# Kernel tuning notes

Hardware: AMD Instinct MI355X
Metric: run time of the kernel (lower is better)

Reference implementation:

```python
import jax, jax.numpy as jnp
import numpy as np

B, T, S_ENC, D, H, E, K = 4, 1024, 64, 1024, 16, 8, 2
DK = D // H
HID = 4 * D
NEG = -65504.0
EPS = 1e-5


def rmsnorm(x, w):
    return w * (x * jax.lax.rsqrt(jnp.mean(x * x, axis=-1, keepdims=True) + EPS))


def mha(xq, xk, xv, mask, wq, wk, wv, wo):
    # linear (no bias): y = x @ W.T
    q = jnp.einsum('bsd,ed->bse', xq, wq).reshape(xq.shape[0], -1, H, DK).transpose(0, 2, 1, 3)
    k = jnp.einsum('bsd,ed->bse', xk, wk).reshape(xk.shape[0], -1, H, DK).transpose(0, 2, 1, 3)
    v = jnp.einsum('bsd,ed->bse', xv, wv).reshape(xv.shape[0], -1, H, DK).transpose(0, 2, 1, 3)
    scores = jnp.einsum('bhqd,bhkd->bhqk', q, k) / jnp.sqrt(jnp.float32(DK))
    scores = jnp.where(mask[:, None, :, :] == 0, NEG, scores)
    attn = jax.nn.softmax(scores, axis=-1)
    out = jnp.einsum('bhqk,bhkd->bhqd', attn, v)
    out = out.transpose(0, 2, 1, 3).reshape(xq.shape[0], -1, D)
    return jnp.einsum('bsd,ed->bse', out, wo)


def moe_ffn(x, gate_w, exp_w1, exp_w2, sh_w1, sh_w2):
    b, s, d = x.shape
    xf = x.reshape(-1, d)                                     # [N, D]
    # shared expert
    sh = jnp.einsum('nd,hd->nh', xf, sh_w1)
    sh = jax.nn.silu(sh)
    sh = jnp.einsum('nh,dh->nd', sh, sh_w2)
    # gating
    logits = jnp.einsum('nd,ed->ne', xf, gate_w)              # [N, E]
    topk_vals, topk_idx = jax.lax.top_k(logits, K)
    topk_gates = jax.nn.softmax(topk_vals, axis=-1)
    n = xf.shape[0]
    gates = jnp.zeros((n, E), dtype=xf.dtype).at[jnp.arange(n)[:, None], topk_idx].set(topk_gates)
    # all experts computed densely (as in the torch code), then gated
    h = jnp.einsum('nd,ehd->neh', xf, exp_w1)                 # [N, E, 4D]
    h = jax.nn.silu(h)
    eo = jnp.einsum('neh,edh->ned', h, exp_w2)                # [N, E, D]
    sel = jnp.einsum('ned,ne->nd', eo, gates)
    return (sh + sel).reshape(b, s, d)


def setup_inputs() -> dict:
    key = jax.random.key(0)
    ks = jax.random.split(key, 16)
    sd = 1.0 / np.sqrt(D)
    inp = {
        'x': jax.random.normal(ks[0], (B, T, D), jnp.float32),
        'encoder_output': jax.random.normal(ks[1], (B, S_ENC, D), jnp.float32),
        'tgt_mask': jnp.tril(jnp.ones((T, T), jnp.int32))[None].repeat(B, 0),
        'src_mask': jnp.ones((B, T, S_ENC), jnp.int32),
        'norm1_w': jnp.ones((D,), jnp.float32),
        'norm2_w': jnp.ones((D,), jnp.float32),
        'norm3_w': jnp.ones((D,), jnp.float32),
        'sa_wq': jax.random.normal(ks[2], (D, D), jnp.float32) * sd,
        'sa_wk': jax.random.normal(ks[3], (D, D), jnp.float32) * sd,
        'sa_wv': jax.random.normal(ks[4], (D, D), jnp.float32) * sd,
        'sa_wo': jax.random.normal(ks[5], (D, D), jnp.float32) * sd,
        'ca_wq': jax.random.normal(ks[6], (D, D), jnp.float32) * sd,
        'ca_wk': jax.random.normal(ks[7], (D, D), jnp.float32) * sd,
        'ca_wv': jax.random.normal(ks[8], (D, D), jnp.float32) * sd,
        'ca_wo': jax.random.normal(ks[9], (D, D), jnp.float32) * sd,
        'gate_w': jax.random.normal(ks[10], (E, D), jnp.float32) * 0.02,
        'exp_w1': jax.random.normal(ks[11], (E, HID, D), jnp.float32) * sd,
        'exp_w2': jax.random.normal(ks[12], (E, D, HID), jnp.float32) / np.sqrt(HID),
        'sh_w1': jax.random.normal(ks[13], (HID, D), jnp.float32) * sd,
        'sh_w2': jax.random.normal(ks[14], (D, HID), jnp.float32) / np.sqrt(HID),
    }
    return inp


def reference(x, encoder_output, tgt_mask, src_mask, norm1_w, norm2_w, norm3_w,
              sa_wq, sa_wk, sa_wv, sa_wo, ca_wq, ca_wk, ca_wv, ca_wo,
              gate_w, exp_w1, exp_w2, sh_w1, sh_w2):
    xn = rmsnorm(x, norm1_w)
    h = x + mha(xn, xn, xn, tgt_mask, sa_wq, sa_wk, sa_wv, sa_wo)
    hn = rmsnorm(h, norm2_w)
    h = h + mha(hn, encoder_output, encoder_output, src_mask, ca_wq, ca_wk, ca_wv, ca_wo)
    hn = rmsnorm(h, norm3_w)
    return h + moe_ffn(hn, gate_w, exp_w1, exp_w2, sh_w1, sh_w2)
```

## Files before the change

kernel.cpp:

```cpp
#include <hip/hip_runtime.h>
#include <hip/hip_bf16.h>
#include <cstdint>
#include <cstddef>
#include <math.h>

typedef __attribute__((ext_vector_type(8))) short bf16x8;
typedef __attribute__((ext_vector_type(4))) float f32x4;
typedef __attribute__((ext_vector_type(4))) short s16x4;

static __device__ __forceinline__ short f2bf(float f) {
  union { __hip_bfloat16 b; short s; } u;
  u.b = __float2bfloat16(f);
  return u.s;
}

static __device__ __forceinline__ float bf2f(short s) {
  union { unsigned u; float f; } v;
  v.u = ((unsigned)(unsigned short)s) << 16;
  return v.f;
}

static __device__ __forceinline__ void gload_lds16(const short* g, short* l) {
  __builtin_amdgcn_global_load_lds((const __attribute__((address_space(1))) void*)g,
                                   (__attribute__((address_space(3))) void*)l,
                                   16, 0, 0);
}

__global__ __launch_bounds__(256) void cvt_k(const float* __restrict__ src,
                                             short* __restrict__ dst, long n4) {
  long i = (long)blockIdx.x * blockDim.x + threadIdx.x;
  long stride = (long)gridDim.x * blockDim.x;
  for (; i < n4; i += stride) {
    float4 v = ((const float4*)src)[i];
    s16x4 o;
    o.x = f2bf(v.x); o.y = f2bf(v.y); o.z = f2bf(v.z); o.w = f2bf(v.w);
    ((s16x4*)dst)[i] = o;
  }
}

__global__ __launch_bounds__(256) void cvt2_k(const float* __restrict__ src,
                                              short* __restrict__ hi,
                                              short* __restrict__ lo, long n4) {
  long i = (long)blockIdx.x * blockDim.x + threadIdx.x;
  long stride = (long)gridDim.x * blockDim.x;
  for (; i < n4; i += stride) {
    float4 v = ((const float4*)src)[i];
    s16x4 h, l;
    h.x = f2bf(v.x); l.x = f2bf(v.x - bf2f(h.x));
    h.y = f2bf(v.y); l.y = f2bf(v.y - bf2f(h.y));
    h.z = f2bf(v.z); l.z = f2bf(v.z - bf2f(h.z));
    h.w = f2bf(v.w); l.w = f2bf(v.w - bf2f(h.w));
    ((s16x4*)hi)[i] = h;
    ((s16x4*)lo)[i] = l;
  }
}

__global__ __launch_bounds__(256) void rms2_k(const float* __restrict__ x,
                                              const float* __restrict__ w,
                                              short* __restrict__ hi,
                                              short* __restrict__ lo) {
  const int row = blockIdx.x, tid = threadIdx.x;
  const float* xr = x + (size_t)row * 1024;
  float4 v = *(const float4*)&xr[tid * 4];
  float ss = v.x * v.x + v.y * v.y + v.z * v.z + v.w * v.w;
#pragma unroll
  for (int off = 32; off; off >>= 1) ss += __shfl_down(ss, off);
  __shared__ float red[4];
  if ((tid & 63) == 0) red[tid >> 6] = ss;
  __syncthreads();
  float rs = rsqrtf((red[0] + red[1] + red[2] + red[3]) * (1.f / 1024.f) + 1e-5f);
  float4 wv = *(const float4*)&w[tid * 4];
  float o0 = v.x * rs * wv.x, o1 = v.y * rs * wv.y;
  float o2 = v.z * rs * wv.z, o3 = v.w * rs * wv.w;
  s16x4 h, l;
  h.x = f2bf(o0); l.x = f2bf(o0 - bf2f(h.x));
  h.y = f2bf(o1); l.y = f2bf(o1 - bf2f(h.y));
  h.z = f2bf(o2); l.z = f2bf(o2 - bf2f(h.z));
  h.w = f2bf(o3); l.w = f2bf(o3 - bf2f(h.w));
  const size_t ib = (size_t)row * 1024 + tid * 4;
  *(s16x4*)&hi[ib] = h;
  *(s16x4*)&lo[ib] = l;
}

__global__ __launch_bounds__(256) void rms_k(const float* __restrict__ x,
                                             const float* __restrict__ w,
                                             short* __restrict__ obf) {
  const int row = blockIdx.x, tid = threadIdx.x;
  const float* xr = x + (size_t)row * 1024;
  float4 v = *(const float4*)&xr[tid * 4];
  float ss = v.x * v.x + v.y * v.y + v.z * v.z + v.w * v.w;
#pragma unroll
  for (int off = 32; off; off >>= 1) ss += __shfl_down(ss, off);
  __shared__ float red[4];
  if ((tid & 63) == 0) red[tid >> 6] = ss;
  __syncthreads();
  float rs = rsqrtf((red[0] + red[1] + red[2] + red[3]) * (1.f / 1024.f) + 1e-5f);
  float4 wv = *(const float4*)&w[tid * 4];
  s16x4 ob;
  ob.x = f2bf(v.x * rs * wv.x); ob.y = f2bf(v.y * rs * wv.y);
  ob.z = f2bf(v.z * rs * wv.z); ob.w = f2bf(v.w * rs * wv.w);
  *(s16x4*)&obf[(size_t)row * 1024 + tid * 4] = ob;
}

template <int EPI>
__global__ __launch_bounds__(256)
void gemm3_k(const short* __restrict__ Ah, const short* __restrict__ Al,
             const short* __restrict__ Bh, const short* __restrict__ Bl,
             float* __restrict__ C, const float* __restrict__ resid,
             int M, int N, int K) {
  __shared__ short sAh[128 * 32];
  __shared__ short sAl[128 * 32];
  __shared__ short sBh[128 * 32];
  __shared__ short sBl[128 * 32];

  const int tid = threadIdx.x;
  const int bn = blockIdx.x, bm = blockIdx.y;
  const int lane = tid & 63, wv = tid >> 6;
  const int rch = lane >> 2, cch = (lane & 3) << 3;
  const int wr = wv >> 1, wc = wv & 1;
  const int lr = lane & 15, lg = lane >> 4;
  const int c0 = wv * 2, c1 = wv * 2 + 1;

  const int ra0 = bm * 128 + c0 * 16 + rch;
  const int ra1 = bm * 128 + c1 * 16 + rch;
  const int rb0 = bn * 128 + c0 * 16 + rch, rb1 = bn * 128 + c1 * 16 + rch;

  f32x4 acc[4][4];
#pragma unroll
  for (int m = 0; m < 4; m++)
#pragma unroll
    for (int n = 0; n < 4; n++) acc[m][n] = (f32x4){0.f, 0.f, 0.f, 0.f};

  const int nk = K >> 5;
  for (int kt = 0; kt < nk; ++kt) {
    __syncthreads();
    const int colk = (kt << 5) + cch;
    gload_lds16(Ah + (size_t)ra0 * K + colk, &sAh[c0 * 512]);
    gload_lds16(Ah + (size_t)ra1 * K + colk, &sAh[c1 * 512]);
    gload_lds16(Al + (size_t)ra0 * K + colk, &sAl[c0 * 512]);
    gload_lds16(Al + (size_t)ra1 * K + colk, &sAl[c1 * 512]);
    gload_lds16(Bh + (size_t)rb0 * K + colk, &sBh[c0 * 512]);
    gload_lds16(Bh + (size_t)rb1 * K + colk, &sBh[c1 * 512]);
    gload_lds16(Bl + (size_t)rb0 * K + colk, &sBl[c0 * 512]);
    gload_lds16(Bl + (size_t)rb1 * K + colk, &sBl[c1 * 512]);
    __syncthreads();
    bf16x8 ah[4], al[4], bh[4], bl[4];
#pragma unroll
    for (int m = 0; m < 4; m++) {
      const int o = (wr * 64 + m * 16 + lr) * 32 + lg * 8;
      ah[m] = *(const bf16x8*)&sAh[o];
      al[m] = *(const bf16x8*)&sAl[o];
    }
#pragma unroll
    for (int n = 0; n < 4; n++) {
      const int o = (wc * 64 + n * 16 + lr) * 32 + lg * 8;
      bh[n] = *(const bf16x8*)&sBh[o];
      bl[n] = *(const bf16x8*)&sBl[o];
    }
#pragma unroll
    for (int m = 0; m < 4; m++)
#pragma unroll
      for (int n = 0; n < 4; n++) {
        acc[m][n] = __builtin_amdgcn_mfma_f32_16x16x32_bf16(ah[m], bh[n], acc[m][n], 0, 0, 0);
        acc[m][n] = __builtin_amdgcn_mfma_f32_16x16x32_bf16(al[m], bh[n], acc[m][n], 0, 0, 0);
        acc[m][n] = __builtin_amdgcn_mfma_f32_16x16x32_bf16(ah[m], bl[n], acc[m][n], 0, 0, 0);
      }
  }

  const int cbase = bn * 128 + wc * 64;
#pragma unroll
  for (int m = 0; m < 4; m++) {
    const int rl = bm * 128 + wr * 64 + m * 16 + lg * 4;
#pragma unroll
    for (int n = 0; n < 4; n++) {
      f32x4 v = acc[m][n];
      const int col = cbase + n * 16 + lr;
#pragma unroll
      for (int j = 0; j < 4; j++) {
        const size_t idx = (size_t)(rl + j) * N + col;
        if (EPI == 0) C[idx] = v[j];
        else C[idx] = v[j] + resid[idx];
      }
    }
  }
}

__global__ __launch_bounds__(256)
void attn32t_k(const float* __restrict__ Q, int ldq,
               const float* __restrict__ K, int ldk,
               const float* __restrict__ V, int ldv,
               short* __restrict__ Oh, short* __restrict__ Ol, int ldo,
               int Tq, int Tkv, int causal, float scale) {
  __shared__ float sQt[64][68];
  __shared__ float sKP[64][68];
  __shared__ float sV[64][68];

  const int idx = blockIdx.x;
  const int qb = 15 - (idx >> 6);
  const int h = (idx >> 2) & 15;
  const int b = idx & 3;
  const int tid = threadIdx.x;
  const int tx = tid & 15, ty = tid >> 4;
  const int hoff = h * 64;
  const int srow = tid >> 2;
  const int scol = (tid & 3) * 4;

  {
    const float* qp = &Q[(size_t)(b * Tq + qb * 64 + srow) * ldq + hoff + scol];
#pragma unroll
    for (int j = 0; j < 4; j++) {
      float4 v = *(const float4*)&qp[j * 16];
      sQt[scol + j * 16 + 0][srow] = v.x;
      sQt[scol + j * 16 + 1][srow] = v.y;
      sQt[scol + j * 16 + 2][srow] = v.z;
      sQt[scol + j * 16 + 3][srow] = v.w;
    }
  }

  float o[4][4];
  float m_run[4], l_run[4];
#pragma unroll
  for (int i = 0; i < 4; i++) {
    m_run[i] = -1e30f; l_run[i] = 0.f;
#pragma unroll
    for (int j = 0; j < 4; j++) o[i][j] = 0.f;
  }

  const int ntiles = causal ? (qb + 1) : (Tkv >> 6);
  for (int kt = 0; kt < ntiles; ++kt) {
    __syncthreads();
    {
      const float* kp = &K[(size_t)(b * Tkv + kt * 64 + srow) * ldk + hoff + scol];
      const float* vp = &V[(size_t)(b * Tkv + kt * 64 + srow) * ldv + hoff + scol];
#pragma unroll
      for (int j = 0; j < 4; j++) {
        float4 kv = *(const float4*)&kp[j * 16];
        sKP[scol + j * 16 + 0][srow] = kv.x;
        sKP[scol + j * 16 + 1][srow] = kv.y;
        sKP[scol + j * 16 + 2][srow] = kv.z;
        sKP[scol + j * 16 + 3][srow] = kv.w;
        *(float4*)&sV[srow][scol + j * 16] = *(const float4*)&vp[j * 16];
      }
    }
    __syncthreads();

    float s[4][4];
#pragma unroll
    for (int i = 0; i < 4; i++)
#pragma unroll
      for (int j = 0; j < 4; j++) s[i][j] = 0.f;
#pragma unroll 2
    for (int d = 0; d < 64; d++) {
      float4 qv = *(const float4*)&sQt[d][ty * 4];
      float4 kv = *(const float4*)&sKP[d][tx * 4];
      float qa[4] = {qv.x, qv.y, qv.z, qv.w};
      float ka[4] = {kv.x, kv.y, kv.z, kv.w};
#pragma unroll
      for (int i = 0; i < 4; i++)
#pragma unroll
        for (int j = 0; j < 4; j++) s[i][j] += qa[i] * ka[j];
    }

#pragma unroll
    for (int i = 0; i < 4; i++) {
      const int qg = qb * 64 + ty * 4 + i;
      float tmax = -1e30f;
#pragma unroll
      for (int j = 0; j < 4; j++) {
        float xv = s[i][j] * scale;
        if (causal && (kt * 64 + tx * 4 + j) > qg) xv = -1e30f;
        s[i][j] = xv;
        tmax = fmaxf(tmax, xv);
      }
      tmax = fmaxf(tmax, __shfl_xor(tmax, 1));
      tmax = fmaxf(tmax, __shfl_xor(tmax, 2));
      tmax = fmaxf(tmax, __shfl_xor(tmax, 4));
      tmax = fmaxf(tmax, __shfl_xor(tmax, 8));
      const float m_new = fmaxf(m_run[i], tmax);
      const float alpha = __expf(m_run[i] - m_new);
      float tsum = 0.f;
#pragma unroll
      for (int j = 0; j < 4; j++) {
        float e = (s[i][j] <= -1e29f) ? 0.f : __expf(s[i][j] - m_new);
        s[i][j] = e; tsum += e;
      }
      tsum += __shfl_xor(tsum, 1);
      tsum += __shfl_xor(tsum, 2);
      tsum += __shfl_xor(tsum, 4);
      tsum += __shfl_xor(tsum, 8);
      l_run[i] = l_run[i] * alpha + tsum;
      m_run[i] = m_new;
#pragma unroll
      for (int j = 0; j < 4; j++) o[i][j] *= alpha;
    }
    __syncthreads();

#pragma unroll
    for (int i = 0; i < 4; i++) {
      float4 pw; pw.x = s[i][0]; pw.y = s[i][1]; pw.z = s[i][2]; pw.w = s[i][3];
      *(float4*)&sKP[ty * 4 + i][tx * 4] = pw;
    }
    __syncthreads();

#pragma unroll 2
    for (int k4 = 0; k4 < 16; k4++) {
      float4 pv[4];
#pragma unroll
      for (int i = 0; i < 4; i++) pv[i] = *(const float4*)&sKP[ty * 4 + i][k4 * 4];
#pragma unroll
      for (int kk = 0; kk < 4; kk++) {
        float4 vv = *(const float4*)&sV[k4 * 4 + kk][tx * 4];
#pragma unroll
        for (int i = 0; i < 4; i++) {
          const float pk = ((const float*)&pv[i])[kk];
          o[i][0] += pk * vv.x; o[i][1] += pk * vv.y;
          o[i][2] += pk * vv.z; o[i][3] += pk * vv.w;
        }
      }
    }
  }

#pragma unroll
  for (int i = 0; i < 4; i++) {
    const float inv = 1.f / l_run[i];
    const size_t ob = (size_t)(b * Tq + qb * 64 + ty * 4 + i) * ldo + hoff + tx * 4;
    s16x4 hh, ll;
    float v0 = o[i][0] * inv, v1 = o[i][1] * inv, v2 = o[i][2] * inv, v3 = o[i][3] * inv;
    hh.x = f2bf(v0); ll.x = f2bf(v0 - bf2f(hh.x));
    hh.y = f2bf(v1); ll.y = f2bf(v1 - bf2f(hh.y));
    hh.z = f2bf(v2); ll.z = f2bf(v2 - bf2f(hh.z));
    hh.w = f2bf(v3); ll.w = f2bf(v3 - bf2f(hh.w));
    *(s16x4*)&Oh[ob] = hh;
    *(s16x4*)&Ol[ob] = ll;
  }
}

template <int EPI, int MODE>
__global__ __launch_bounds__(256)
void gemm_bt_k(const short* __restrict__ A, const short* __restrict__ B,
               void* C, int M, int N, int K,
               const int* __restrict__ row_map,
               const int* __restrict__ counts,
               const int* __restrict__ offs) {
  __shared__ short sA[128 * 32];
  __shared__ short sB[128 * 32];
  __shared__ int sRow[128];

  const int tid = threadIdx.x;
  const int bn = blockIdx.x, bm = blockIdx.y;
  const int e = blockIdx.z;
  const int cnt = counts[e];
  const int base = offs[e];
  if (bm * 128 >= cnt) return;
  const short* Bp = B + (size_t)e * N * K;

  const int lane = tid & 63, wv = tid >> 6;
  const int rch = lane >> 2, cch = (lane & 3) << 3;
  const int wr = wv >> 1, wc = wv & 1;
  const int lr = lane & 15, lg = lane >> 4;
  const int c0 = wv * 2, c1 = wv * 2 + 1;

  int ra0, ra1;
  if (MODE == 2) {
    int rl0 = bm * 128 + c0 * 16 + rch, rl1 = bm * 128 + c1 * 16 + rch;
    ra0 = base + ((rl0 < cnt) ? rl0 : 0);
    ra1 = base + ((rl1 < cnt) ? rl1 : 0);
  } else {
    if (tid < 128) {
      int r = bm * 128 + tid;
      sRow[tid] = (r < cnt) ? row_map[base + r] : row_map[base];
    }
    __syncthreads();
    ra0 = sRow[c0 * 16 + rch];
    ra1 = sRow[c1 * 16 + rch];
  }
  const int rb0 = bn * 128 + c0 * 16 + rch, rb1 = bn * 128 + c1 * 16 + rch;

  f32x4 acc[4][4];
#pragma unroll
  for (int m = 0; m < 4; m++)
#pragma unroll
    for (int n = 0; n < 4; n++) acc[m][n] = (f32x4){0.f, 0.f, 0.f, 0.f};

  const int nk = K >> 5;
  for (int kt = 0; kt < nk; ++kt) {
    __syncthreads();
    const int colk = (kt << 5) + cch;
    gload_lds16(A + (size_t)ra0 * K + colk, &sA[c0 * 512]);
    gload_lds16(A + (size_t)ra1 * K + colk, &sA[c1 * 512]);
    gload_lds16(Bp + (size_t)rb0 * K + colk, &sB[c0 * 512]);
    gload_lds16(Bp + (size_t)rb1 * K + colk, &sB[c1 * 512]);
    __syncthreads();
    bf16x8 a[4], b[4];
#pragma unroll
    for (int m = 0; m < 4; m++) a[m] = *(const bf16x8*)&sA[(wr * 64 + m * 16 + lr) * 32 + lg * 8];
#pragma unroll
    for (int n = 0; n < 4; n++) b[n] = *(const bf16x8*)&sB[(wc * 64 + n * 16 + lr) * 32 + lg * 8];
#pragma unroll
    for (int m = 0; m < 4; m++)
#pragma unroll
      for (int n = 0; n < 4; n++)
        acc[m][n] = __builtin_amdgcn_mfma_f32_16x16x32_bf16(a[m], b[n], acc[m][n], 0, 0, 0);
  }

  const int cbase = bn * 128 + wc * 64;
#pragma unroll
  for (int m = 0; m < 4; m++) {
    const int rl = wr * 64 + m * 16 + lg * 4;
#pragma unroll
    for (int n = 0; n < 4; n++) {
      f32x4 v = acc[m][n];
      const int col = cbase + n * 16 + lr;
#pragma unroll
      for (int j = 0; j < 4; j++) {
        const int rloc = bm * 128 + rl + j;
        if (rloc >= cnt) continue;
        const size_t idx = (size_t)(base + rloc) * N + col;
        float xv = v[j];
        if (EPI == 1) {
          float s = xv / (1.f + __expf(-xv));
          ((short*)C)[idx] = f2bf(s);
        } else {
          ((float*)C)[idx] = xv;
        }
      }
    }
  }
}

__global__ __launch_bounds__(256) void gate_k(const float* __restrict__ H,
                                              const float* __restrict__ w3,
                                              const float* __restrict__ gw,
                                              int* counts, int* tok_e, int* tok_s,
                                              float* tok_g) {
  const int token = blockIdx.x * 4 + (threadIdx.x >> 6);
  const int lane = threadIdx.x & 63;
  const float* xr = H + (size_t)token * 1024;
  double a[8] = {0, 0, 0, 0, 0, 0, 0, 0};
  double ss = 0.0;
#pragma unroll
  for (int i = 0; i < 4; i++) {
    float4 xv = *(const float4*)&xr[i * 256 + lane * 4];
    float4 w3v = *(const float4*)&w3[i * 256 + lane * 4];
    ss += (double)xv.x * xv.x + (double)xv.y * xv.y + (double)xv.z * xv.z + (double)xv.w * xv.w;
    double xw0 = (double)xv.x * (double)w3v.x, xw1 = (double)xv.y * (double)w3v.y;
    double xw2 = (double)xv.z * (double)w3v.z, xw3 = (double)xv.w * (double)w3v.w;
#pragma unroll
    for (int e = 0; e < 8; e++) {
      float4 wv = *(const float4*)&gw[e * 1024 + i * 256 + lane * 4];
      a[e] += xw0 * wv.x + xw1 * wv.y + xw2 * wv.z + xw3 * wv.w;
    }
  }
#pragma unroll
  for (int off = 32; off; off >>= 1) {
    ss += __shfl_down(ss, off);
#pragma unroll
    for (int e = 0; e < 8; e++) a[e] += __shfl_down(a[e], off);
  }
  if (lane == 0) {
    double v0 = a[0]; int i0 = 0;
#pragma unroll
    for (int e = 1; e < 8; e++) if (a[e] > v0) { v0 = a[e]; i0 = e; }
    double v1 = -1e300; int i1 = 0;
#pragma unroll
    for (int e = 0; e < 8; e++) if (e != i0 && a[e] > v1) { v1 = a[e]; i1 = e; }
    double rs = 1.0 / sqrt(ss * (1.0 / 1024.0) + 1e-5);
    double t = exp((v1 - v0) * rs);
    double g0 = 1.0 / (1.0 + t);
    int s0 = atomicAdd(&counts[i0], 1);
    int s1 = atomicAdd(&counts[i1], 1);
    tok_e[2 * token] = i0; tok_e[2 * token + 1] = i1;
    tok_s[2 * token] = s0; tok_s[2 * token + 1] = s1;
    tok_g[2 * token] = (float)g0; tok_g[2 * token + 1] = (float)(1.0 - g0);
  }
}

__global__ void offsets_k(int* counts, int* offs) {
  if (threadIdx.x == 0 && blockIdx.x == 0) {
    counts[8] = 4096;
    int s = 0;
    for (int e = 0; e < 9; e++) { offs[e] = s; s += counts[e]; }
  }
}

__global__ __launch_bounds__(256) void build_rows_k(const int* __restrict__ offs,
                                                    const int* __restrict__ tok_e,
                                                    const int* __restrict__ tok_s,
                                                    int* __restrict__ row_map,
                                                    int* __restrict__ tok_row) {
  int n = blockIdx.x * 256 + threadIdx.x;
  int e0 = tok_e[2 * n], e1 = tok_e[2 * n + 1];
  int r0 = offs[e0] + tok_s[2 * n], r1 = offs[e1] + tok_s[2 * n + 1];
  row_map[r0] = n; row_map[r1] = n;
  row_map[8192 + n] = n;
  tok_row[2 * n] = r0; tok_row[2 * n + 1] = r1;
}

__global__ __launch_bounds__(256) void combine_k(const float* __restrict__ H,
                                                 const float* __restrict__ eo,
                                                 const int* __restrict__ tok_row,
                                                 const float* __restrict__ tok_g,
                                                 float* __restrict__ out) {
  const int n = blockIdx.x, t = threadIdx.x;
  const int r0 = tok_row[2 * n], r1 = tok_row[2 * n + 1];
  const float g0 = tok_g[2 * n], g1 = tok_g[2 * n + 1];
  const size_t ib = (size_t)n * 1024 + t * 4;
  float4 hv = *(const float4*)&H[ib];
  float4 sv = *(const float4*)&eo[(size_t)(8192 + n) * 1024 + t * 4];
  float4 a0 = *(const float4*)&eo[(size_t)r0 * 1024 + t * 4];
  float4 a1 = *(const float4*)&eo[(size_t)r1 * 1024 + t * 4];
  float4 ov;
  ov.x = hv.x + sv.x + g0 * a0.x + g1 * a1.x;
  ov.y = hv.y + sv.y + g0 * a0.y + g1 * a1.y;
  ov.z = hv.z + sv.z + g0 * a0.z + g1 * a1.z;
  ov.w = hv.w + sv.w + g0 * a0.w + g1 * a1.w;
  *(float4*)&out[ib] = ov;
}

extern "C" void kernel_launch(void* const* d_in, const int* in_sizes, int n_in,
                              void* d_out, int out_size, void* d_ws, size_t ws_size,
                              hipStream_t stream) {
  (void)in_sizes; (void)n_in; (void)out_size;
  const float* x     = (const float*)d_in[0];
  const float* enc   = (const float*)d_in[1];
  const float* n1w   = (const float*)d_in[4];
  const float* n2w   = (const float*)d_in[5];
  const float* n3w   = (const float*)d_in[6];
  const float* sa_wq = (const float*)d_in[7];
  const float* sa_wk = (const float*)d_in[8];
  const float* sa_wv = (const float*)d_in[9];
  const float* sa_wo = (const float*)d_in[10];
  const float* ca_wq = (const float*)d_in[11];
  const float* ca_wk = (const float*)d_in[12];
  const float* ca_wv = (const float*)d_in[13];
  const float* ca_wo = (const float*)d_in[14];
  const float* gw    = (const float*)d_in[15];
  const float* e_w1  = (const float*)d_in[16];
  const float* e_w2  = (const float*)d_in[17];
  const float* s_w1  = (const float*)d_in[18];
  const float* s_w2  = (const float*)d_in[19];
  float* out = (float*)d_out;

  char* p = (char*)d_ws;
  size_t off = 0;
  auto alloc = [&](size_t bytes) -> void* {
    void* r = p + off;
    off += (bytes + 255) & ~(size_t)255;
    return r;
  };
  short* w_all1 = (short*)alloc(9LL * 4096 * 1024 * 2);
  short* w_all2 = (short*)alloc(9LL * 1024 * 4096 * 2);
  short* xn     = (short*)alloc(4096LL * 1024 * 2);
  char*  U      = (char*)alloc(12288LL * 4096 * 2);
  float* qkvb   = (float*)U;
  short* hbuf   = (short*)U;
  float* Hb     = (float*)alloc(4096LL * 1024 * 4);
  float* eo     = (float*)alloc(12288LL * 1024 * 4);
  short* xh     = (short*)alloc(4096LL * 1024 * 2);
  short* xl     = (short*)alloc(4096LL * 1024 * 2);
  short* ench   = (short*)alloc(256LL * 1024 * 2);
  short* encl   = (short*)alloc(256LL * 1024 * 2);
  short* wsh    = (short*)alloc(3072LL * 1024 * 2);
  short* wsl    = (short*)alloc(3072LL * 1024 * 2);
  int*   counts = (int*)alloc(9 * 4);
  int*   offs   = (int*)alloc(9 * 4);
  int*   tok_e  = (int*)alloc(4096LL * 2 * 4);
  int*   tok_s  = (int*)alloc(4096LL * 2 * 4);
  float* tok_g  = (float*)alloc(4096LL * 2 * 4);
  int*   tok_row= (int*)alloc(4096LL * 2 * 4);
  int*   row_map= (int*)alloc(12288LL * 4);
  if (off > ws_size) return;

  float* crossQ = qkvb;
  float* encKV  = qkvb + 8388608;

  auto cvt = [&](const float* s, short* d, long n) {
    long n4 = n / 4;
    long g = (n4 + 255) / 256;
    int grid = (int)(g > 4096 ? 4096 : g);
    cvt_k<<<grid, 256, 0, stream>>>(s, d, n4);
  };
  auto cvt2 = [&](const float* s, short* h, short* l, long n) {
    long n4 = n / 4;
    long g = (n4 + 255) / 256;
    int grid = (int)(g > 4096 ? 4096 : g);
    cvt2_k<<<grid, 256, 0, stream>>>(s, h, l, n4);
  };

  cvt(e_w1, w_all1, 8L * 4096 * 1024);
  cvt(s_w1, w_all1 + 8L * 4096 * 1024, 4096L * 1024);
  cvt(e_w2, w_all2, 8L * 1024 * 4096);
  cvt(s_w2, w_all2 + 8L * 1024 * 4096, 1024L * 4096);
  cvt2(enc, ench, encl, 256L * 1024);

  rms2_k<<<4096, 256, 0, stream>>>(x, n1w, xh, xl);
  cvt2(sa_wq, wsh, wsl, 1024L * 1024);
  cvt2(sa_wk, wsh + 1048576, wsl + 1048576, 1024L * 1024);
  cvt2(sa_wv, wsh + 2097152, wsl + 2097152, 1024L * 1024);
  gemm3_k<0><<<dim3(24, 32), 256, 0, stream>>>(xh, xl, wsh, wsl, qkvb, nullptr,
      4096, 3072, 1024);
  attn32t_k<<<1024, 256, 0, stream>>>(qkvb, 3072, qkvb + 1024, 3072, qkvb + 2048, 3072,
      xh, xl, 1024, 1024, 1024, 1, 0.125f);
  cvt2(sa_wo, wsh, wsl, 1024L * 1024);
  gemm3_k<2><<<dim3(8, 32), 256, 0, stream>>>(xh, xl, wsh, wsl, Hb, x,
      4096, 1024, 1024);

  rms2_k<<<4096, 256, 0, stream>>>(Hb, n2w, xh, xl);
  cvt2(ca_wq, wsh, wsl, 1024L * 1024);
  gemm3_k<0><<<dim3(8, 32), 256, 0, stream>>>(xh, xl, wsh, wsl, crossQ, nullptr,
      4096, 1024, 1024);
  cvt2(ca_wk, wsh, wsl, 1024L * 1024);
  cvt2(ca_wv, wsh + 1048576, wsl + 1048576, 1024L * 1024);
  gemm3_k<0><<<dim3(16, 2), 256, 0, stream>>>(ench, encl, wsh, wsl, encKV, nullptr,
      256, 2048, 1024);
  attn32t_k<<<1024, 256, 0, stream>>>(crossQ, 1024, encKV, 2048, encKV + 1024, 2048,
      xh, xl, 1024, 1024, 64, 0, 0.125f);
  cvt2(ca_wo, wsh, wsl, 1024L * 1024);
  gemm3_k<2><<<dim3(8, 32), 256, 0, stream>>>(xh, xl, wsh, wsl, Hb, Hb,
      4096, 1024, 1024);

  rms_k<<<4096, 256, 0, stream>>>(Hb, n3w, xn);
  hipMemsetAsync(counts, 0, 8 * sizeof(int), stream);
  gate_k<<<1024, 256, 0, stream>>>(Hb, n3w, gw, counts, tok_e, tok_s, tok_g);
  offsets_k<<<1, 1, 0, stream>>>(counts, offs);
  build_rows_k<<<16, 256, 0, stream>>>(offs, tok_e, tok_s, row_map, tok_row);
  gemm_bt_k<1, 1><<<dim3(32, 32, 9), 256, 0, stream>>>(xn, w_all1, hbuf,
      4096, 4096, 1024, row_map, counts, offs);
  gemm_bt_k<3, 2><<<dim3(8, 32, 9), 256, 0, stream>>>(hbuf, w_all2, eo,
      4096, 1024, 4096, nullptr, counts, offs);

  combine_k<<<4096, 256, 0, stream>>>(Hb, eo, tok_row, tok_g, out);
}
```

Before: 1.075 ms.

## Move attention onto split-bf16 MFMA and add XCD-aware workgroup swizzle to GEMMs

Replaces the fp32 scalar FMA attention kernel with an MFMA version that keeps Q, K, V and P as bf16 hi/lo pairs and uses three MFMAs per product. The QKV and cross-Q/KV GEMMs now write hi/lo bf16 directly instead of fp32, which halves the intermediate traffic. All GEMM launches become 1D grids, with the block index remapped so neighbouring tiles land on the same XCD for L2 reuse. The split-bf16 scheme aims to keep near-fp32 accuracy but adds extra MFMA work and LDS staging.

Result: slower. 1.331 ms (+23.8%).

```diff
diff --git a/kernel.cpp b/kernel.cpp
--- a/kernel.cpp
+++ b/kernel.cpp
@@ -24,6 +24,12 @@
   __builtin_amdgcn_global_load_lds((const __attribute__((address_space(1))) void*)g,
                                    (__attribute__((address_space(3))) void*)l,
                                    16, 0, 0);
+}
+
+static __device__ __forceinline__ int xcd_swizzle(int orig, int nwg) {
+  int q = nwg >> 3, r = nwg & 7;
+  int xcd = orig & 7, loc = orig >> 3;
+  return (xcd < r ? xcd * (q + 1) : r * (q + 1) + (xcd - r) * q) + loc;
 }
 
 __global__ __launch_bounds__(256) void cvt_k(const float* __restrict__ src,
@@ -107,14 +113,16 @@
 void gemm3_k(const short* __restrict__ Ah, const short* __restrict__ Al,
              const short* __restrict__ Bh, const short* __restrict__ Bl,
              float* __restrict__ C, const float* __restrict__ resid,
-             int M, int N, int K) {
+             short* __restrict__ Ch, short* __restrict__ Cl,
+             int M, int N, int K, int nbn) {
   __shared__ short sAh[128 * 32];
   __shared__ short sAl[128 * 32];
   __shared__ short sBh[128 * 32];
   __shared__ short sBl[128 * 32];
 
+  const int wgid = xcd_swizzle(blockIdx.x, gridDim.x);
+  const int bm = wgid / nbn, bn = wgid % nbn;
   const int tid = threadIdx.x;
-  const int bn = blockIdx.x, bm = blockIdx.y;
   const int lane = tid & 63, wv = tid >> 6;
   const int rch = lane >> 2, cch = (lane & 3) << 3;
   const int wr = wv >> 1, wc = wv & 1;
@@ -178,160 +186,175 @@
 #pragma unroll
       for (int j = 0; j < 4; j++) {
         const size_t idx = (size_t)(rl + j) * N + col;
-        if (EPI == 0) C[idx] = v[j];
-        else C[idx] = v[j] + resid[idx];
+        if (EPI == 0) {
+          C[idx] = v[j];
+        } else if (EPI == 2) {
+          C[idx] = v[j] + resid[idx];
+        } else {
+          short hh = f2bf(v[j]);
+          Ch[idx] = hh;
+          Cl[idx] = f2bf(v[j] - bf2f(hh));
+        }
       }
     }
   }
 }
 
+template <bool CAUSAL>
 __global__ __launch_bounds__(256)
-void attn32t_k(const float* __restrict__ Q, int ldq,
-               const float* __restrict__ K, int ldk,
-               const float* __restrict__ V, int ldv,
-               short* __restrict__ Oh, short* __restrict__ Ol, int ldo,
-               int Tq, int Tkv, int causal, float scale) {
-  __shared__ float sQt[64][68];
-  __shared__ float sKP[64][68];
-  __shared__ float sV[64][68];
+void attn3_k(const short* __restrict__ Qh, const short* __restrict__ Ql, int ldq,
+             const short* __restrict__ Kh, const short* __restrict__ Kl, int ldk,
+             const short* __restrict__ Vh, const short* __restrict__ Vl, int ldv,
+             short* __restrict__ Oh, short* __restrict__ Ol, int ldo,
+             int Tq, int Tkv, float scale) {
+  __shared__ short sQh[64 * 64], sQl[64 * 64];
+  __shared__ short sKh[64 * 64], sKl[64 * 64];
+  __shared__ short sVh[64 * 72], sVl[64 * 72];
+  __shared__ short sPh[4][16 * 72], sPl[4][16 * 72];
 
   const int idx = blockIdx.x;
   const int qb = 15 - (idx >> 6);
   const int h = (idx >> 2) & 15;
   const int b = idx & 3;
-  const int tid = threadIdx.x;
-  const int tx = tid & 15, ty = tid >> 4;
+  const int tid = threadIdx.x, lane = tid & 63, wv = tid >> 6;
   const int hoff = h * 64;
-  const int srow = tid >> 2;
-  const int scol = (tid & 3) * 4;
-
-  {
-    const float* qp = &Q[(size_t)(b * Tq + qb * 64 + srow) * ldq + hoff + scol];
-#pragma unroll
-    for (int j = 0; j < 4; j++) {
-      float4 v = *(const float4*)&qp[j * 16];
-      sQt[scol + j * 16 + 0][srow] = v.x;
-      sQt[scol + j * 16 + 1][srow] = v.y;
-      sQt[scol + j * 16 + 2][srow] = v.z;
-      sQt[scol + j * 16 + 3][srow] = v.w;
-    }
-  }
-
-  float o[4][4];
-  float m_run[4], l_run[4];
-#pragma unroll
-  for (int i = 0; i < 4; i++) {
-    m_run[i] = -1e30f; l_run[i] = 0.f;
-#pragma unroll
-    for (int j = 0; j < 4; j++) o[i][j] = 0.f;
-  }
-
-  const int ntiles = causal ? (qb + 1) : (Tkv >> 6);
+  const int lr = lane & 15, lg = lane >> 4;
+  const int qlo = wv * 16;
+
+#pragma unroll
+  for (int j = 0; j < 2; j++) {
+    int c = j * 256 + tid;
+    int row = c >> 3, col = (c & 7) << 3;
+    size_t g = (size_t)(b * Tq + qb * 64 + row) * ldq + hoff + col;
+    *(bf16x8*)&sQh[row * 64 + col] = *(const bf16x8*)&Qh[g];
+    *(bf16x8*)&sQl[row * 64 + col] = *(const bf16x8*)&Ql[g];
+  }
+
+  float m_run = -1e30f, l_run = 0.f;
+  f32x4 o[4];
+#pragma unroll
+  for (int n = 0; n < 4; n++) o[n] = (f32x4){0.f, 0.f, 0.f, 0.f};
+
+  const int ntiles = CAUSAL ? (qb + 1) : (Tkv >> 6);
   for (int kt = 0; kt < ntiles; ++kt) {
     __syncthreads();
-    {
-      const float* kp = &K[(size_t)(b * Tkv + kt * 64 + srow) * ldk + hoff + scol];
-      const float* vp = &V[(size_t)(b * Tkv + kt * 64 + srow) * ldv + hoff + scol];
-#pragma unroll
-      for (int j = 0; j < 4; j++) {
-        float4 kv = *(const float4*)&kp[j * 16];
-        sKP[scol + j * 16 + 0][srow] = kv.x;
-        sKP[scol + j * 16 + 1][srow] = kv.y;
-        sKP[scol + j * 16 + 2][srow] = kv.z;
-        sKP[scol + j * 16 + 3][srow] = kv.w;
-        *(float4*)&sV[srow][scol + j * 16] = *(const float4*)&vp[j * 16];
+#pragma unroll
+    for (int j = 0; j < 2; j++) {
+      int c = j * 256 + tid;
+      int row = c >> 3, col = (c & 7) << 3;
+      size_t gk = (size_t)(b * Tkv + kt * 64 + row) * ldk + hoff + col;
+      *(bf16x8*)&sKh[row * 64 + col] = *(const bf16x8*)&Kh[gk];
+      *(bf16x8*)&sKl[row * 64 + col] = *(const bf16x8*)&Kl[gk];
+      size_t gv = (size_t)(b * Tkv + kt * 64 + row) * ldv + hoff + col;
+      bf16x8 vh = *(const bf16x8*)&Vh[gv];
+      bf16x8 vl = *(const bf16x8*)&Vl[gv];
+#pragma unroll
+      for (int i = 0; i < 8; i++) {
+        sVh[(col + i) * 72 + row] = vh[i];
+        sVl[(col + i) * 72 + row] = vl[i];
       }
     }
     __syncthreads();
 
-    float s[4][4];
-#pragma unroll
-    for (int i = 0; i < 4; i++)
-#pragma unroll
-      for (int j = 0; j < 4; j++) s[i][j] = 0.f;
-#pragma unroll 2
-    for (int d = 0; d < 64; d++) {
-      float4 qv = *(const float4*)&sQt[d][ty * 4];
-      float4 kv = *(const float4*)&sKP[d][tx * 4];
-      float qa[4] = {qv.x, qv.y, qv.z, qv.w};
-      float ka[4] = {kv.x, kv.y, kv.z, kv.w};
-#pragma unroll
-      for (int i = 0; i < 4; i++)
-#pragma unroll
-        for (int j = 0; j < 4; j++) s[i][j] += qa[i] * ka[j];
-    }
-
-#pragma unroll
-    for (int i = 0; i < 4; i++) {
-      const int qg = qb * 64 + ty * 4 + i;
-      float tmax = -1e30f;
-#pragma unroll
-      for (int j = 0; j < 4; j++) {
-        float xv = s[i][j] * scale;
-        if (causal && (kt * 64 + tx * 4 + j) > qg) xv = -1e30f;
-        s[i][j] = xv;
+    f32x4 st[4];
+#pragma unroll
+    for (int jk = 0; jk < 4; jk++) st[jk] = (f32x4){0.f, 0.f, 0.f, 0.f};
+#pragma unroll
+    for (int ks = 0; ks < 2; ks++) {
+      bf16x8 qh = *(const bf16x8*)&sQh[(qlo + lr) * 64 + ks * 32 + lg * 8];
+      bf16x8 ql = *(const bf16x8*)&sQl[(qlo + lr) * 64 + ks * 32 + lg * 8];
+#pragma unroll
+      for (int jk = 0; jk < 4; jk++) {
+        const int o2 = (jk * 16 + lr) * 64 + ks * 32 + lg * 8;
+        bf16x8 kh = *(const bf16x8*)&sKh[o2];
+        bf16x8 kl = *(const bf16x8*)&sKl[o2];
+        st[jk] = __builtin_amdgcn_mfma_f32_16x16x32_bf16(kh, qh, st[jk], 0, 0, 0);
+        st[jk] = __builtin_amdgcn_mfma_f32_16x16x32_bf16(kl, qh, st[jk], 0, 0, 0);
+        st[jk] = __builtin_amdgcn_mfma_f32_16x16x32_bf16(kh, ql, st[jk], 0, 0, 0);
+      }
+    }
+
+    const int qg = qb * 64 + qlo + lr;
+    float s[16];
+    float tmax = -1e30f;
+#pragma unroll
+    for (int jk = 0; jk < 4; jk++)
+#pragma unroll
+      for (int r2 = 0; r2 < 4; r2++) {
+        float xv = st[jk][r2] * scale;
+        if (CAUSAL && kt == qb) {
+          int kvidx = kt * 64 + jk * 16 + lg * 4 + r2;
+          if (kvidx > qg) xv = -1e30f;
+        }
+        s[jk * 4 + r2] = xv;
         tmax = fmaxf(tmax, xv);
       }
-      tmax = fmaxf(tmax, __shfl_xor(tmax, 1));
-      tmax = fmaxf(tmax, __shfl_xor(tmax, 2));
-      tmax = fmaxf(tmax, __shfl_xor(tmax, 4));
-      tmax = fmaxf(tmax, __shfl_xor(tmax, 8));
-      const float m_new = fmaxf(m_run[i], tmax);
-      const float alpha = __expf(m_run[i] - m_new);
-      float tsum = 0.f;
-#pragma unroll
-      for (int j = 0; j < 4; j++) {
-        float e = (s[i][j] <= -1e29f) ? 0.f : __expf(s[i][j] - m_new);
-        s[i][j] = e; tsum += e;
+    tmax = fmaxf(tmax, __shfl_xor(tmax, 16));
+    tmax = fmaxf(tmax, __shfl_xor(tmax, 32));
+    float m_new = fmaxf(m_run, tmax);
+    float alpha = __expf(m_run - m_new);
+    float tsum = 0.f;
+#pragma unroll
+    for (int i = 0; i < 16; i++) {
+      float ev = (s[i] <= -1e29f) ? 0.f : __expf(s[i] - m_new);
+      s[i] = ev;
+      tsum += ev;
+    }
+    tsum += __shfl_xor(tsum, 16);
+    tsum += __shfl_xor(tsum, 32);
+    l_run = l_run * alpha + tsum;
+    m_run = m_new;
+
+    short* pwh = &sPh[wv][0];
+    short* pwl = &sPl[wv][0];
+#pragma unroll
+    for (int jk = 0; jk < 4; jk++) {
+      s16x4 ph, pl;
+      float e0 = s[jk * 4 + 0], e1 = s[jk * 4 + 1], e2 = s[jk * 4 + 2], e3 = s[jk * 4 + 3];
+      ph.x = f2bf(e0); pl.x = f2bf(e0 - bf2f(ph.x));
+      ph.y = f2bf(e1); pl.y = f2bf(e1 - bf2f(ph.y));
+      ph.z = f2bf(e2); pl.z = f2bf(e2 - bf2f(ph.z));
+      ph.w = f2bf(e3); pl.w = f2bf(e3 - bf2f(ph.w));
+      *(s16x4*)&pwh[lr * 72 + jk * 16 + lg * 4] = ph;
+      *(s16x4*)&pwl[lr * 72 + jk * 16 + lg * 4] = pl;
+    }
+#pragma unroll
+    for (int r2 = 0; r2 < 4; r2++) {
+      float al = __shfl(alpha, lg * 4 + r2);
+#pragma unroll
+      for (int db = 0; db < 4; db++) o[db][r2] *= al;
+    }
+    __syncthreads();
+
+#pragma unroll
+    for (int ks = 0; ks < 2; ks++) {
+      bf16x8 pah = *(const bf16x8*)&pwh[lr * 72 + ks * 32 + lg * 8];
+      bf16x8 pal = *(const bf16x8*)&pwl[lr * 72 + ks * 32 + lg * 8];
+#pragma unroll
+      for (int db = 0; db < 4; db++) {
+        const int o2 = (db * 16 + lr) * 72 + ks * 32 + lg * 8;
+        bf16x8 vfh = *(const bf16x8*)&sVh[o2];
+        bf16x8 vfl = *(const bf16x8*)&sVl[o2];
+        o[db] = __builtin_amdgcn_mfma_f32_16x16x32_bf16(pah, vfh, o[db], 0, 0, 0);
+        o[db] = __builtin_amdgcn_mfma_f32_16x16x32_bf16(pal, vfh, o[db], 0, 0, 0);
+        o[db] = __builtin_amdgcn_mfma_f32_16x16x32_bf16(pah, vfl, o[db], 0, 0, 0);
       }
-      tsum += __shfl_xor(tsum, 1);
-      tsum += __shfl_xor(tsum, 2);
-      tsum += __shfl_xor(tsum, 4);
-      tsum += __shfl_xor(tsum, 8);
-      l_run[i] = l_run[i] * alpha + tsum;
-      m_run[i] = m_new;
-#pragma unroll
-      for (int j = 0; j < 4; j++) o[i][j] *= alpha;
-    }
-    __syncthreads();
-
-#pragma unroll
-    for (int i = 0; i < 4; i++) {
-      float4 pw; pw.x = s[i][0]; pw.y = s[i][1]; pw.z = s[i][2]; pw.w = s[i][3];
-      *(float4*)&sKP[ty * 4 + i][tx * 4] = pw;
-    }
-    __syncthreads();
-
-#pragma unroll 2
-    for (int k4 = 0; k4 < 16; k4++) {
-      float4 pv[4];
-#pragma unroll
-      for (int i = 0; i < 4; i++) pv[i] = *(const float4*)&sKP[ty * 4 + i][k4 * 4];
-#pragma unroll
-      for (int kk = 0; kk < 4; kk++) {
-        float4 vv = *(const float4*)&sV[k4 * 4 + kk][tx * 4];
-#pragma unroll
-        for (int i = 0; i < 4; i++) {
-          const float pk = ((const float*)&pv[i])[kk];
-          o[i][0] += pk * vv.x; o[i][1] += pk * vv.y;
-          o[i][2] += pk * vv.z; o[i][3] += pk * vv.w;
-        }
-      }
-    }
-  }
-
-#pragma unroll
-  for (int i = 0; i < 4; i++) {
-    const float inv = 1.f / l_run[i];
-    const size_t ob = (size_t)(b * Tq + qb * 64 + ty * 4 + i) * ldo + hoff + tx * 4;
-    s16x4 hh, ll;
-    float v0 = o[i][0] * inv, v1 = o[i][1] * inv, v2 = o[i][2] * inv, v3 = o[i][3] * inv;
-    hh.x = f2bf(v0); ll.x = f2bf(v0 - bf2f(hh.x));
-    hh.y = f2bf(v1); ll.y = f2bf(v1 - bf2f(hh.y));
-    hh.z = f2bf(v2); ll.z = f2bf(v2 - bf2f(hh.z));
-    hh.w = f2bf(v3); ll.w = f2bf(v3 - bf2f(hh.w));
-    *(s16x4*)&Oh[ob] = hh;
-    *(s16x4*)&Ol[ob] = ll;
+    }
+  }
+
+  float rinv = 1.f / l_run;
+#pragma unroll
+  for (int r2 = 0; r2 < 4; r2++) {
+    float inv = __shfl(rinv, lg * 4 + r2);
+    int token = b * Tq + qb * 64 + qlo + lg * 4 + r2;
+#pragma unroll
+    for (int db = 0; db < 4; db++) {
+      float vv = o[db][r2] * inv;
+      short hh = f2bf(vv);
+      const size_t ob = (size_t)token * ldo + hoff + db * 16 + lr;
+      Oh[ob] = hh;
+      Ol[ob] = f2bf(vv - bf2f(hh));
+    }
   }
 }
 
@@ -341,14 +364,19 @@
                void* C, int M, int N, int K,
                const int* __restrict__ row_map,
                const int* __restrict__ counts,
-               const int* __restrict__ offs) {
+               const int* __restrict__ offs,
+               int nbn, int nbm) {
   __shared__ short sA[128 * 32];
   __shared__ short sB[128 * 32];
   __shared__ int sRow[128];
 
+  const int wgid = xcd_swizzle(blockIdx.x, gridDim.x);
+  const int per = nbn * nbm;
+  const int e = wgid / per;
+  const int rem = wgid % per;
+  const int bm = rem / nbn, bn = rem % nbn;
+
   const int tid = threadIdx.x;
-  const int bn = blockIdx.x, bm = blockIdx.y;
-  const int e = blockIdx.z;
   const int cnt = counts[e];
   const int base = offs[e];
   if (bm * 128 >= cnt) return;
@@ -552,7 +580,6 @@
   short* w_all2 = (short*)alloc(9LL * 1024 * 4096 * 2);
   short* xn     = (short*)alloc(4096LL * 1024 * 2);
   char*  U      = (char*)alloc(12288LL * 4096 * 2);
-  float* qkvb   = (float*)U;
   short* hbuf   = (short*)U;
   float* Hb     = (float*)alloc(4096LL * 1024 * 4);
   float* eo     = (float*)alloc(12288LL * 1024 * 4);
@@ -571,8 +598,12 @@
   int*   row_map= (int*)alloc(12288LL * 4);
   if (off > ws_size) return;
 
-  float* crossQ = qkvb;
-  float* encKV  = qkvb + 8388608;
+  short* qkvh = (short*)U;
+  short* qkvl = qkvh + 4096LL * 3072;
+  short* crossQh = (short*)U;
+  short* crossQl = crossQh + 4096LL * 1024;
+  short* encKVh  = crossQl + 4096LL * 1024;
+  short* encKVl  = encKVh + 256LL * 2048;
 
   auto cvt = [&](const float* s, short* d, long n) {
     long n4 = n / 4;
@@ -597,37 +628,39 @@
   cvt2(sa_wq, wsh, wsl, 1024L * 1024);
   cvt2(sa_wk, wsh + 1048576, wsl + 1048576, 1024L * 1024);
   cvt2(sa_wv, wsh + 2097152, wsl + 2097152, 1024L * 1024);
-  gemm3_k<0><<<dim3(24, 32), 256, 0, stream>>>(xh, xl, wsh, wsl, qkvb, nullptr,
-      4096, 3072, 1024);
-  attn32t_k<<<1024, 256, 0, stream>>>(qkvb, 3072, qkvb + 1024, 3072, qkvb + 2048, 3072,
-      xh, xl, 1024, 1024, 1024, 1, 0.125f);
+  gemm3_k<3><<<768, 256, 0, stream>>>(xh, xl, wsh, wsl, nullptr, nullptr,
+      qkvh, qkvl, 4096, 3072, 1024, 24);
+  attn3_k<true><<<1024, 256, 0, stream>>>(qkvh, qkvl, 3072,
+      qkvh + 1024, qkvl + 1024, 3072, qkvh + 2048, qkvl + 2048, 3072,
+      xh, xl, 1024, 1024, 1024, 0.125f);
   cvt2(sa_wo, wsh, wsl, 1024L * 1024);
-  gemm3_k<2><<<dim3(8, 32), 256, 0, stream>>>(xh, xl, wsh, wsl, Hb, x,
-      4096, 1024, 1024);
+  gemm3_k<2><<<256, 256, 0, stream>>>(xh, xl, wsh, wsl, Hb, x,
+      nullptr, nullptr, 4096, 1024, 1024, 8);
 
   rms2_k<<<4096, 256, 0, stream>>>(Hb, n2w, xh, xl);
   cvt2(ca_wq, wsh, wsl, 1024L * 1024);
-  gemm3_k<0><<<dim3(8, 32), 256, 0, stream>>>(xh, xl, wsh, wsl, crossQ, nullptr,
-      4096, 1024, 1024);
+  gemm3_k<3><<<256, 256, 0, stream>>>(xh, xl, wsh, wsl, nullptr, nullptr,
+      crossQh, crossQl, 4096, 1024, 1024, 8);
   cvt2(ca_wk, wsh, wsl, 1024L * 1024);
   cvt2(ca_wv, wsh + 1048576, wsl + 1048576, 1024L * 1024);
-  gemm3_k<0><<<dim3(16, 2), 256, 0, stream>>>(ench, encl, wsh, wsl, encKV, nullptr,
-      256, 2048, 1024);
-  attn32t_k<<<1024, 256, 0, stream>>>(crossQ, 1024, encKV, 2048, encKV + 1024, 2048,
-      xh, xl, 1024, 1024, 64, 0, 0.125f);
+  gemm3_k<3><<<32, 256, 0, stream>>>(ench, encl, wsh, wsl, nullptr, nullptr,
+      encKVh, encKVl, 256, 2048, 1024, 16);
+  attn3_k<false><<<1024, 256, 0, stream>>>(crossQh, crossQl, 1024,
+      encKVh, encKVl, 2048, encKVh + 1024, encKVl + 1024, 2048,
+      xh, xl, 1024, 1024, 64, 0.125f);
   cvt2(ca_wo, wsh, wsl, 1024L * 1024);
-  gemm3_k<2><<<dim3(8, 32), 256, 0, stream>>>(xh, xl, wsh, wsl, Hb, Hb,
-      4096, 1024, 1024);
+  gemm3_k<2><<<256, 256, 0, stream>>>(xh, xl, wsh, wsl, Hb, Hb,
+      nullptr, nullptr, 4096, 1024, 1024, 8);
 
   rms_k<<<4096, 256, 0, stream>>>(Hb, n3w, xn);
   hipMemsetAsync(counts, 0, 8 * sizeof(int), stream);
   gate_k<<<1024, 256, 0, stream>>>(Hb, n3w, gw, counts, tok_e, tok_s, tok_g);
   offsets_k<<<1, 1, 0, stream>>>(counts, offs);
   build_rows_k<<<16, 256, 0, stream>>>(offs, tok_e, tok_s, row_map, tok_row);
-  gemm_bt_k<1, 1><<<dim3(32, 32, 9), 256, 0, stream>>>(xn, w_all1, hbuf,
-      4096, 4096, 1024, row_map, counts, offs);
-  gemm_bt_k<3, 2><<<dim3(8, 32, 9), 256, 0, stream>>>(hbuf, w_all2, eo,
-      4096, 1024, 4096, nullptr, counts, offs);
+  gemm_bt_k<1, 1><<<9216, 256, 0, stream>>>(xn, w_all1, hbuf,
+      4096, 4096, 1024, row_map, counts, offs, 32, 32);
+  gemm_bt_k<3, 2><<<2304, 256, 0, stream>>>(hbuf, w_all2, eo,
+      4096, 1024, 4096, nullptr, counts, offs, 8, 32);
 
   combine_k<<<4096, 256, 0, stream>>>(Hb, eo, tok_row, tok_g, out);
 }
```
